# Optimization experiments

Hardware: AMD Instinct MI355X
Metric: run time of the kernel (lower is better)

Reference implementation:

```python
import jax, jax.numpy as jnp
import numpy as np

SEQ, B, IN, H, L = 512, 64, 128, 256, 6
STDV = 1.0 / (H ** 0.5)


def setup_inputs() -> dict:
    key = jax.random.key(0)
    ks = jax.random.split(key, 7)
    return {
        "x": jax.random.normal(ks[0], (SEQ, B, IN), jnp.float32),
        "h0": jax.random.normal(ks[1], (L, B, H), jnp.float32),
        "w_ih0": jax.random.uniform(ks[2], (3 * H, IN), jnp.float32, -STDV, STDV),
        "w_ih_rest": jax.random.uniform(ks[3], (L - 1, 3 * H, H), jnp.float32, -STDV, STDV),
        "w_hh": jax.random.uniform(ks[4], (L, 3 * H, H), jnp.float32, -STDV, STDV),
        "b_ih": jax.random.uniform(ks[5], (L, 3 * H), jnp.float32, -STDV, STDV),
        "b_hh": jax.random.uniform(ks[6], (L, 3 * H), jnp.float32, -STDV, STDV),
    }


def _gru_layer(x, h0, w_ih, w_hh, b_ih, b_hh):
    # Precompute input-side gate projections for all timesteps: (S, B, 3H)
    xg = jnp.einsum("sbi,gi->sbg", x, w_ih) + b_ih

    def step(h, xg_t):
        hg = h @ w_hh.T + b_hh  # (B, 3H)
        xr, xz, xn = jnp.split(xg_t, 3, axis=-1)
        hr, hz, hn = jnp.split(hg, 3, axis=-1)
        r = jax.nn.sigmoid(xr + hr)
        z = jax.nn.sigmoid(xz + hz)
        n = jnp.tanh(xn + r * hn)
        h_new = (1.0 - z) * n + z * h
        return h_new, h_new

    h_n, ys = jax.lax.scan(step, h0, xg)
    return ys, h_n


def reference(x, h0, w_ih0, w_ih_rest, w_hh, b_ih, b_hh):
    cur = x
    h_finals = []
    for i in range(L):
        w_ih = w_ih0 if i == 0 else w_ih_rest[i - 1]
        cur, h_n = _gru_layer(cur, h0[i], w_ih, w_hh[i], b_ih[i], b_hh[i])
        h_finals.append(h_n)
    return cur, jnp.stack(h_finals, axis=0)
```

## Files before the change

kernel.cpp:

```cpp
#include <hip/hip_runtime.h>

#define SEQ 512
#define BB 64
#define IN_DIM 128
#define HH 256
#define NL 6
#define G3 768
#define KT 16
#define SA 520
#define CUS_PER_LAYER 16
#define JPC 16
#define RD 4
#define RING_ELEMS (BB*HH)

typedef short short8 __attribute__((ext_vector_type(8)));
typedef short short4v __attribute__((ext_vector_type(4)));
typedef float f32x4 __attribute__((ext_vector_type(4)));

#define FLAGS_OFF_B (NL*RD*RING_ELEMS*2)
#define NFLAG_INTS  (NL*16 + 16)

__device__ __forceinline__ short f2bf(float f) {
    unsigned u = __builtin_bit_cast(unsigned, f);
    u += 0x7fffu + ((u >> 16) & 1u);
    return (short)(u >> 16);
}
__device__ __forceinline__ float sigm(float v) { return __fdividef(1.f, 1.f + __expf(-v)); }
__device__ __forceinline__ float tanh_f(float v) { float e = __expf(2.f * v); return 1.f - __fdividef(2.f, e + 1.f); }

__global__ __launch_bounds__(256, 1) void gru_persist(
    const float* __restrict__ x, const float* __restrict__ h0,
    const float* __restrict__ w_ih0, const float* __restrict__ w_ih_rest,
    const float* __restrict__ w_hh, const float* __restrict__ b_ih,
    const float* __restrict__ b_hh, float* __restrict__ y,
    short* __restrict__ ring, int* __restrict__ flags)
{
    extern __shared__ char dynpad[];
    (void)dynpad;

    const int tid = threadIdx.x;
    const unsigned long long ddl = __builtin_amdgcn_s_memrealtime() + 1000000000ull;

    const int xcc = __builtin_amdgcn_s_getreg(20 | (31 << 11)) & 0xf;
    if (xcc >= NL) return;
    __shared__ int s_slot;
    int* tickets = flags + NL * 16;
    if (tid == 0) s_slot = __hip_atomic_fetch_add(&tickets[xcc], 1, __ATOMIC_RELAXED, __HIP_MEMORY_SCOPE_AGENT);
    __syncthreads();
    const int slot = s_slot;
    if (slot >= CUS_PER_LAYER) return;

    const int l = xcc;
    const int jbase = slot * JPC;
    const int lane = tid & 63;
    const int wave = tid >> 6;
    const int q = lane >> 4;
    const int jj = lane & 15;
    const int jrow = jbase + jj;

    #define SQF(L) (flags + (L) * 16)

    __shared__ short sAm[64 * SA];
    __shared__ float sH[64 * 17];

    short* ring_init = ring + (l * RD + 3) * RING_ELEMS;
    for (int i = tid; i < BB * JPC; i += 256) {
        int b = i >> 4, j2 = i & 15;
        float v = h0[(size_t)l * BB * HH + b * HH + jbase + j2];
        sH[b * 17 + j2] = v;
        ring_init[b * HH + jbase + j2] = f2bf(v);
    }
    __syncthreads();
    if (tid == 0)
        __hip_atomic_store(&SQF(l)[slot], 1, __ATOMIC_RELEASE, __HIP_MEMORY_SCOPE_AGENT);

    if (l == 0) {
        short8 z8 = {};
        for (int i = tid; i < 64 * 16; i += 256) {
            int row = i >> 4, c8 = (i & 15) * 8;
            *reinterpret_cast<short8*>(&sAm[row * SA + 384 + c8]) = z8;
        }
    }

    const int KIN = (l == 0) ? IN_DIM : HH;
    const float* wih = (l == 0) ? w_ih0 : (w_ih_rest + (size_t)(l - 1) * G3 * HH);
    const float* whh = w_hh + (size_t)l * G3 * HH;
    const int kq = q * 8;
    short8 Breg[3 * KT];
    #pragma unroll
    for (int g = 0; g < 3; ++g) {
        const int row = g * HH + jrow;
        #pragma unroll
        for (int kt = 0; kt < KT; ++kt) {
            int k = kt * 32 + kq;
            short8 v = {};
            const float* p = nullptr;
            if (k < KIN)            p = wih + (size_t)row * KIN + k;
            else if (k < KIN + HH)  p = whh + (size_t)row * HH + (k - KIN);
            if (p) {
                float4 a = *(const float4*)p;
                float4 c = *(const float4*)(p + 4);
                v[0] = f2bf(a.x); v[1] = f2bf(a.y); v[2] = f2bf(a.z); v[3] = f2bf(a.w);
                v[4] = f2bf(c.x); v[5] = f2bf(c.y); v[6] = f2bf(c.z); v[7] = f2bf(c.w);
            }
            Breg[g * KT + kt] = v;
        }
    }
    const float bsr = b_ih[l * G3 + jrow] + b_hh[l * G3 + jrow];
    const float bsz = b_ih[l * G3 + HH + jrow] + b_hh[l * G3 + HH + jrow];
    const float bin_ = b_ih[l * G3 + 2 * HH + jrow];
    const float bhn_ = b_hh[l * G3 + 2 * HH + jrow];

    const int ksplit = (l == 0) ? 4 : 8;
    const int Mbase = wave * 16;
    const int aoff = (Mbase + jj) * SA + kq;

    int* paddr = SQF(l) + jj;
    bool pactive = false;
    int tshift = 0;
    if (wave == 0) {
        if (q == 0)      { paddr = SQF(l) + jj;     tshift = 1;  pactive = true; }
        else if (q == 1) { if (l > 0)      { paddr = SQF(l - 1) + jj; tshift = 2;  pactive = true; } }
        else if (q == 2) { if (l < NL - 1) { paddr = SQF(l + 1) + jj; tshift = -2; pactive = true; } }
    }

    for (int t = 0; t < SEQ; ++t) {
        if (wave == 0) {
            const int target = t + tshift;
            int iter = 0;
            for (;;) {
                int v = __hip_atomic_load(paddr, __ATOMIC_RELAXED, __HIP_MEMORY_SCOPE_AGENT);
                bool ok = (!pactive) || (v >= target);
                if (__ballot(ok) == 0xFFFFFFFFFFFFFFFFull) break;
                if (((++iter) & 63) == 0 && __builtin_amdgcn_s_memrealtime() > ddl) break;
            }
            __builtin_amdgcn_fence(__ATOMIC_ACQUIRE, "agent");
        }
        __syncthreads();

        {
            const short8* ph = (const short8*)((const char*)(ring + (l * RD + ((t + 3) & 3)) * RING_ELEMS) + tid * 128);
            short8 h0v = ph[0], h1v = ph[1], h2v = ph[2], h3v = ph[3];
            short8 h4v = ph[4], h5v = ph[5], h6v = ph[6], h7v = ph[7];
            short* dh = &sAm[(tid >> 2) * SA + KIN + (tid & 3) * 64];
            if (l == 0) {
                const float* xt = x + (size_t)t * BB * IN_DIM;
                #pragma unroll
                for (int i = 0; i < 8; ++i) {
                    int c = tid + i * 256;
                    int row = c >> 5, col = (c & 31) * 4;
                    float4 vv = *(const float4*)(xt + row * IN_DIM + col);
                    short4v s;
                    s[0] = f2bf(vv.x); s[1] = f2bf(vv.y); s[2] = f2bf(vv.z); s[3] = f2bf(vv.w);
                    *reinterpret_cast<short4v*>(&sAm[row * SA + col]) = s;
                }
            } else {
                const short8* pf = (const short8*)((const char*)(ring + ((l - 1) * RD + (t & 3)) * RING_ELEMS) + tid * 128);
                short8 w0 = pf[0], w1 = pf[1], w2 = pf[2], w3 = pf[3];
                short8 w4 = pf[4], w5 = pf[5], w6 = pf[6], w7 = pf[7];
                short* dx = &sAm[(tid >> 2) * SA + (tid & 3) * 64];
                *(short8*)(dx + 0)  = w0; *(short8*)(dx + 8)  = w1;
                *(short8*)(dx + 16) = w2; *(short8*)(dx + 24) = w3;
                *(short8*)(dx + 32) = w4; *(short8*)(dx + 40) = w5;
                *(short8*)(dx + 48) = w6; *(short8*)(dx + 56) = w7;
            }
            *(short8*)(dh + 0)  = h0v; *(short8*)(dh + 8)  = h1v;
            *(short8*)(dh + 16) = h2v; *(short8*)(dh + 24) = h3v;
            *(short8*)(dh + 32) = h4v; *(short8*)(dh + 40) = h5v;
            *(short8*)(dh + 48) = h6v; *(short8*)(dh + 56) = h7v;
        }
        __syncthreads();

        f32x4 ax0 = {}, ax1 = {}, ax2 = {}, ah0 = {}, ah1 = {}, ah2 = {};
        #pragma unroll
        for (int kt = 0; kt < KT; ++kt) {
            short8 a = *reinterpret_cast<const short8*>(&sAm[aoff + kt * 32]);
            if (kt < ksplit) {
                ax0 = __builtin_amdgcn_mfma_f32_16x16x32_bf16(a, Breg[0 * KT + kt], ax0, 0, 0, 0);
                ax1 = __builtin_amdgcn_mfma_f32_16x16x32_bf16(a, Breg[1 * KT + kt], ax1, 0, 0, 0);
                ax2 = __builtin_amdgcn_mfma_f32_16x16x32_bf16(a, Breg[2 * KT + kt], ax2, 0, 0, 0);
            } else {
                ah0 = __builtin_amdgcn_mfma_f32_16x16x32_bf16(a, Breg[0 * KT + kt], ah0, 0, 0, 0);
                ah1 = __builtin_amdgcn_mfma_f32_16x16x32_bf16(a, Breg[1 * KT + kt], ah1, 0, 0, 0);
                ah2 = __builtin_amdgcn_mfma_f32_16x16x32_bf16(a, Breg[2 * KT + kt], ah2, 0, 0, 0);
            }
        }

        short* rdst = ring + (l * RD + (t & 3)) * RING_ELEMS;
        float* ydst = y + (size_t)t * BB * HH;
        #pragma unroll
        for (int r = 0; r < 4; ++r) {
            int b = Mbase + 4 * q + r;
            float ho = sH[b * 17 + jj];
            float rg = sigm(ax0[r] + ah0[r] + bsr);
            float zg = sigm(ax1[r] + ah1[r] + bsz);
            float ng = tanh_f(ax2[r] + bin_ + rg * (ah2[r] + bhn_));
            float hn = ng + zg * (ho - ng);
            sH[b * 17 + jj] = hn;
            rdst[b * HH + jrow] = f2bf(hn);
            if (l == NL - 1) ydst[b * HH + jrow] = hn;
        }
        __syncthreads();
        if (tid == 0)
            __hip_atomic_store(&SQF(l)[slot], t + 2, __ATOMIC_RELEASE, __HIP_MEMORY_SCOPE_AGENT);
    }

    for (int i = tid; i < BB * JPC; i += 256) {
        int b = i >> 4, j2 = i & 15;
        y[(size_t)SEQ * BB * HH + (size_t)l * BB * HH + b * HH + jbase + j2] = sH[b * 17 + j2];
    }
}

extern "C" void kernel_launch(void* const* d_in, const int* in_sizes, int n_in,
                              void* d_out, int out_size, void* d_ws, size_t ws_size,
                              hipStream_t stream) {
    (void)in_sizes; (void)n_in; (void)out_size; (void)ws_size;
    const float* x         = (const float*)d_in[0];
    const float* h0        = (const float*)d_in[1];
    const float* w_ih0     = (const float*)d_in[2];
    const float* w_ih_rest = (const float*)d_in[3];
    const float* w_hh      = (const float*)d_in[4];
    const float* b_ih      = (const float*)d_in[5];
    const float* b_hh      = (const float*)d_in[6];
    float* y = (float*)d_out;

    short* ring = (short*)d_ws;
    int* flags  = (int*)((char*)d_ws + FLAGS_OFF_B);

    (void)hipMemsetAsync(flags, 0, NFLAG_INTS * sizeof(int), stream);
    gru_persist<<<256, 256, 16384, stream>>>(
        x, h0, w_ih0, w_ih_rest, w_hh, b_ih, b_hh, y, ring, flags);
}
```

Baseline: 4.630 ms.

## Split layers by batch groups with streamed weight fragments and chunked inter-layer handoff

Replaces the per-layer column split (16 CUs each owning 16 hidden units, exchanging the full hidden state every step) with a batch split: 4 CUs per layer each own 16 batch rows and all hidden units. The recurrence then stays local, with no per-timestep cross-CU synchronisation. A prep kernel converts weights into MFMA-fragment-ordered bf16 that each step streams from global/L2 instead of holding them in registers. Layers hand off through a chunked ring of 8 timesteps with producer and consumer flags. Each step now re-reads the full weight set from cache, and fewer CUs are active.

```diff
diff --git a/kernel.cpp b/kernel.cpp
--- a/kernel.cpp
+++ b/kernel.cpp
@@ -6,19 +6,24 @@
 #define HH 256
 #define NL 6
 #define G3 768
-#define KT 16
 #define SA 520
-#define CUS_PER_LAYER 16
-#define JPC 16
-#define RD 4
-#define RING_ELEMS (BB*HH)
+#define GPL 4
+#define MB 16
+#define CHUNK 8
+#define NSLOT 4
 
 typedef short short8 __attribute__((ext_vector_type(8)));
 typedef short short4v __attribute__((ext_vector_type(4)));
 typedef float f32x4 __attribute__((ext_vector_type(4)));
 
-#define FLAGS_OFF_B (NL*RD*RING_ELEMS*2)
-#define NFLAG_INTS  (NL*16 + 16)
+#define L0_FRAGS (48*12)
+#define LN_FRAGS (48*16)
+#define TOT_FRAGS (L0_FRAGS + 5*LN_FRAGS)
+#define STREAM_SHORTS ((size_t)TOT_FRAGS*512)
+#define FR_SLOT_SH ((size_t)CHUNK*MB*HH)
+#define FR_TOTAL_SH ((size_t)5*GPL*NSLOT*FR_SLOT_SH)
+#define FLAGS_OFF_B ((STREAM_SHORTS + FR_TOTAL_SH)*2)
+#define NFLAG_INTS (16 + 2*NL*GPL*16)
 
 __device__ __forceinline__ short f2bf(float f) {
     unsigned u = __builtin_bit_cast(unsigned, f);
@@ -28,186 +33,193 @@
 __device__ __forceinline__ float sigm(float v) { return __fdividef(1.f, 1.f + __expf(-v)); }
 __device__ __forceinline__ float tanh_f(float v) { float e = __expf(2.f * v); return 1.f - __fdividef(2.f, e + 1.f); }
 
-__global__ __launch_bounds__(256, 1) void gru_persist(
+__device__ __forceinline__ void spin1(int* p, int target, unsigned long long ddl) {
+    if (__hip_atomic_load(p, __ATOMIC_RELAXED, __HIP_MEMORY_SCOPE_AGENT) >= target) return;
+    for (;;) {
+        __builtin_amdgcn_s_sleep(2);
+        if (__hip_atomic_load(p, __ATOMIC_RELAXED, __HIP_MEMORY_SCOPE_AGENT) >= target) return;
+        if (__builtin_amdgcn_s_memrealtime() > ddl) return;
+    }
+}
+
+__global__ __launch_bounds__(256) void prep_frags(
+    const float* __restrict__ w_ih0, const float* __restrict__ w_ih_rest,
+    const float* __restrict__ w_hh, short* __restrict__ stream)
+{
+    int id = blockIdx.x * 256 + threadIdx.x;
+    if (id >= TOT_FRAGS * 64) return;
+    int fid = id >> 6, lane = id & 63;
+    int l, rem, KIN;
+    if (fid < L0_FRAGS) { l = 0; rem = fid; KIN = IN_DIM; }
+    else { int z = fid - L0_FRAGS; l = 1 + z / LN_FRAGS; rem = z - (l - 1) * LN_FRAGS; KIN = HH; }
+    int kt = rem / 48, nt = rem % 48;
+    int jt = nt / 3, gate = nt - jt * 3;
+    int jj = lane & 15, q2 = lane >> 4;
+    int row = gate * HH + jt * 16 + jj;
+    int k0 = kt * 32 + q2 * 8;
+    const float* src;
+    if (k0 < KIN) {
+        src = (l == 0) ? (w_ih0 + (size_t)row * IN_DIM + k0)
+                       : (w_ih_rest + (size_t)(l - 1) * G3 * HH + (size_t)row * HH + k0);
+    } else {
+        src = w_hh + (size_t)l * G3 * HH + (size_t)row * HH + (k0 - KIN);
+    }
+    float4 a = *(const float4*)src;
+    float4 c = *(const float4*)(src + 4);
+    short8 v;
+    v[0] = f2bf(a.x); v[1] = f2bf(a.y); v[2] = f2bf(a.z); v[3] = f2bf(a.w);
+    v[4] = f2bf(c.x); v[5] = f2bf(c.y); v[6] = f2bf(c.z); v[7] = f2bf(c.w);
+    *((short8*)stream + (size_t)fid * 64 + lane) = v;
+}
+
+template<int KTL, int KS>
+__device__ __forceinline__ void compute_step(const short* sAm, const short8* bs,
+                                             int wave, int lane, f32x4* acc)
+{
+    const int arow = (lane & 15) * SA + ((lane >> 4) * 8);
+    const int w6 = wave * 6;
+    #pragma unroll
+    for (int kt = 0; kt < KTL; ++kt) {
+        short8 a = *reinterpret_cast<const short8*>(&sAm[arow + kt * 32]);
+        const short8* bp = bs + ((size_t)(kt * 48 + w6) * 64 + lane);
+        short8 b0 = bp[0 * 64], b1 = bp[1 * 64], b2 = bp[2 * 64];
+        short8 b3 = bp[3 * 64], b4 = bp[4 * 64], b5 = bp[5 * 64];
+        acc[0] = __builtin_amdgcn_mfma_f32_16x16x32_bf16(a, b0, acc[0], 0, 0, 0);
+        acc[1] = __builtin_amdgcn_mfma_f32_16x16x32_bf16(a, b1, acc[1], 0, 0, 0);
+        if (kt < KS) acc[2] = __builtin_amdgcn_mfma_f32_16x16x32_bf16(a, b2, acc[2], 0, 0, 0);
+        else         acc[3] = __builtin_amdgcn_mfma_f32_16x16x32_bf16(a, b2, acc[3], 0, 0, 0);
+        acc[4] = __builtin_amdgcn_mfma_f32_16x16x32_bf16(a, b3, acc[4], 0, 0, 0);
+        acc[5] = __builtin_amdgcn_mfma_f32_16x16x32_bf16(a, b4, acc[5], 0, 0, 0);
+        if (kt < KS) acc[6] = __builtin_amdgcn_mfma_f32_16x16x32_bf16(a, b5, acc[6], 0, 0, 0);
+        else         acc[7] = __builtin_amdgcn_mfma_f32_16x16x32_bf16(a, b5, acc[7], 0, 0, 0);
+    }
+}
+
+__global__ __launch_bounds__(512, 1) void gru_persist(
     const float* __restrict__ x, const float* __restrict__ h0,
-    const float* __restrict__ w_ih0, const float* __restrict__ w_ih_rest,
-    const float* __restrict__ w_hh, const float* __restrict__ b_ih,
-    const float* __restrict__ b_hh, float* __restrict__ y,
-    short* __restrict__ ring, int* __restrict__ flags)
+    const float* __restrict__ b_ih, const float* __restrict__ b_hh,
+    float* __restrict__ y, const short* __restrict__ stream,
+    short* __restrict__ fring, int* __restrict__ flags)
 {
-    extern __shared__ char dynpad[];
-    (void)dynpad;
-
+    extern __shared__ short sAm[];
     const int tid = threadIdx.x;
     const unsigned long long ddl = __builtin_amdgcn_s_memrealtime() + 1000000000ull;
 
     const int xcc = __builtin_amdgcn_s_getreg(20 | (31 << 11)) & 0xf;
     if (xcc >= NL) return;
     __shared__ int s_slot;
-    int* tickets = flags + NL * 16;
-    if (tid == 0) s_slot = __hip_atomic_fetch_add(&tickets[xcc], 1, __ATOMIC_RELAXED, __HIP_MEMORY_SCOPE_AGENT);
+    if (tid == 0) s_slot = __hip_atomic_fetch_add(&flags[xcc], 1, __ATOMIC_RELAXED, __HIP_MEMORY_SCOPE_AGENT);
     __syncthreads();
-    const int slot = s_slot;
-    if (slot >= CUS_PER_LAYER) return;
+    const int g = s_slot;
+    if (g >= GPL) return;
 
     const int l = xcc;
-    const int jbase = slot * JPC;
     const int lane = tid & 63;
     const int wave = tid >> 6;
     const int q = lane >> 4;
     const int jj = lane & 15;
-    const int jrow = jbase + jj;
-
-    #define SQF(L) (flags + (L) * 16)
-
-    __shared__ short sAm[64 * SA];
-    __shared__ float sH[64 * 17];
-
-    short* ring_init = ring + (l * RD + 3) * RING_ELEMS;
-    for (int i = tid; i < BB * JPC; i += 256) {
-        int b = i >> 4, j2 = i & 15;
-        float v = h0[(size_t)l * BB * HH + b * HH + jbase + j2];
-        sH[b * 17 + j2] = v;
-        ring_init[b * HH + jbase + j2] = f2bf(v);
-    }
-    __syncthreads();
-    if (tid == 0)
-        __hip_atomic_store(&SQF(l)[slot], 1, __ATOMIC_RELEASE, __HIP_MEMORY_SCOPE_AGENT);
-
-    if (l == 0) {
-        short8 z8 = {};
-        for (int i = tid; i < 64 * 16; i += 256) {
-            int row = i >> 4, c8 = (i & 15) * 8;
-            *reinterpret_cast<short8*>(&sAm[row * SA + 384 + c8]) = z8;
-        }
-    }
-
-    const int KIN = (l == 0) ? IN_DIM : HH;
-    const float* wih = (l == 0) ? w_ih0 : (w_ih_rest + (size_t)(l - 1) * G3 * HH);
-    const float* whh = w_hh + (size_t)l * G3 * HH;
-    const int kq = q * 8;
-    short8 Breg[3 * KT];
+    const int KINC = (l == 0) ? IN_DIM : HH;
+
+    int* seqf  = flags + 16 + (l * GPL + g) * 16;
+    int* cseqf = flags + 16 + NL * GPL * 16 + (l * GPL + g) * 16;
+    int* seq_prev  = flags + 16 + ((l - 1) * GPL + g) * 16;
+    int* cseq_next = flags + 16 + NL * GPL * 16 + ((l + 1) * GPL + g) * 16;
+
+    const short8* bs = (const short8*)stream + (size_t)((l == 0) ? 0 : (L0_FRAGS + (l - 1) * LN_FRAGS)) * 64;
+
+    float hcur[8];
+    float bR[2], bZ[2], bNx[2], bNh[2];
     #pragma unroll
-    for (int g = 0; g < 3; ++g) {
-        const int row = g * HH + jrow;
-        #pragma unroll
-        for (int kt = 0; kt < KT; ++kt) {
-            int k = kt * 32 + kq;
-            short8 v = {};
-            const float* p = nullptr;
-            if (k < KIN)            p = wih + (size_t)row * KIN + k;
-            else if (k < KIN + HH)  p = whh + (size_t)row * HH + (k - KIN);
-            if (p) {
-                float4 a = *(const float4*)p;
-                float4 c = *(const float4*)(p + 4);
-                v[0] = f2bf(a.x); v[1] = f2bf(a.y); v[2] = f2bf(a.z); v[3] = f2bf(a.w);
-                v[4] = f2bf(c.x); v[5] = f2bf(c.y); v[6] = f2bf(c.z); v[7] = f2bf(c.w);
-            }
-            Breg[g * KT + kt] = v;
-        }
-    }
-    const float bsr = b_ih[l * G3 + jrow] + b_hh[l * G3 + jrow];
-    const float bsz = b_ih[l * G3 + HH + jrow] + b_hh[l * G3 + HH + jrow];
-    const float bin_ = b_ih[l * G3 + 2 * HH + jrow];
-    const float bhn_ = b_hh[l * G3 + 2 * HH + jrow];
-
-    const int ksplit = (l == 0) ? 4 : 8;
-    const int Mbase = wave * 16;
-    const int aoff = (Mbase + jj) * SA + kq;
-
-    int* paddr = SQF(l) + jj;
-    bool pactive = false;
-    int tshift = 0;
-    if (wave == 0) {
-        if (q == 0)      { paddr = SQF(l) + jj;     tshift = 1;  pactive = true; }
-        else if (q == 1) { if (l > 0)      { paddr = SQF(l - 1) + jj; tshift = 2;  pactive = true; } }
-        else if (q == 2) { if (l < NL - 1) { paddr = SQF(l + 1) + jj; tshift = -2; pactive = true; } }
-    }
-
-    for (int t = 0; t < SEQ; ++t) {
-        if (wave == 0) {
-            const int target = t + tshift;
-            int iter = 0;
-            for (;;) {
-                int v = __hip_atomic_load(paddr, __ATOMIC_RELAXED, __HIP_MEMORY_SCOPE_AGENT);
-                bool ok = (!pactive) || (v >= target);
-                if (__ballot(ok) == 0xFFFFFFFFFFFFFFFFull) break;
-                if (((++iter) & 63) == 0 && __builtin_amdgcn_s_memrealtime() > ddl) break;
-            }
-            __builtin_amdgcn_fence(__ATOMIC_ACQUIRE, "agent");
-        }
-        __syncthreads();
-
-        {
-            const short8* ph = (const short8*)((const char*)(ring + (l * RD + ((t + 3) & 3)) * RING_ELEMS) + tid * 128);
-            short8 h0v = ph[0], h1v = ph[1], h2v = ph[2], h3v = ph[3];
-            short8 h4v = ph[4], h5v = ph[5], h6v = ph[6], h7v = ph[7];
-            short* dh = &sAm[(tid >> 2) * SA + KIN + (tid & 3) * 64];
-            if (l == 0) {
-                const float* xt = x + (size_t)t * BB * IN_DIM;
-                #pragma unroll
-                for (int i = 0; i < 8; ++i) {
-                    int c = tid + i * 256;
-                    int row = c >> 5, col = (c & 31) * 4;
-                    float4 vv = *(const float4*)(xt + row * IN_DIM + col);
-                    short4v s;
-                    s[0] = f2bf(vv.x); s[1] = f2bf(vv.y); s[2] = f2bf(vv.z); s[3] = f2bf(vv.w);
-                    *reinterpret_cast<short4v*>(&sAm[row * SA + col]) = s;
-                }
-            } else {
-                const short8* pf = (const short8*)((const char*)(ring + ((l - 1) * RD + (t & 3)) * RING_ELEMS) + tid * 128);
-                short8 w0 = pf[0], w1 = pf[1], w2 = pf[2], w3 = pf[3];
-                short8 w4 = pf[4], w5 = pf[5], w6 = pf[6], w7 = pf[7];
-                short* dx = &sAm[(tid >> 2) * SA + (tid & 3) * 64];
-                *(short8*)(dx + 0)  = w0; *(short8*)(dx + 8)  = w1;
-                *(short8*)(dx + 16) = w2; *(short8*)(dx + 24) = w3;
-                *(short8*)(dx + 32) = w4; *(short8*)(dx + 40) = w5;
-                *(short8*)(dx + 48) = w6; *(short8*)(dx + 56) = w7;
-            }
-            *(short8*)(dh + 0)  = h0v; *(short8*)(dh + 8)  = h1v;
-            *(short8*)(dh + 16) = h2v; *(short8*)(dh + 24) = h3v;
-            *(short8*)(dh + 32) = h4v; *(short8*)(dh + 40) = h5v;
-            *(short8*)(dh + 48) = h6v; *(short8*)(dh + 56) = h7v;
-        }
-        __syncthreads();
-
-        f32x4 ax0 = {}, ax1 = {}, ax2 = {}, ah0 = {}, ah1 = {}, ah2 = {};
-        #pragma unroll
-        for (int kt = 0; kt < KT; ++kt) {
-            short8 a = *reinterpret_cast<const short8*>(&sAm[aoff + kt * 32]);
-            if (kt < ksplit) {
-                ax0 = __builtin_amdgcn_mfma_f32_16x16x32_bf16(a, Breg[0 * KT + kt], ax0, 0, 0, 0);
-                ax1 = __builtin_amdgcn_mfma_f32_16x16x32_bf16(a, Breg[1 * KT + kt], ax1, 0, 0, 0);
-                ax2 = __builtin_amdgcn_mfma_f32_16x16x32_bf16(a, Breg[2 * KT + kt], ax2, 0, 0, 0);
-            } else {
-                ah0 = __builtin_amdgcn_mfma_f32_16x16x32_bf16(a, Breg[0 * KT + kt], ah0, 0, 0, 0);
-                ah1 = __builtin_amdgcn_mfma_f32_16x16x32_bf16(a, Breg[1 * KT + kt], ah1, 0, 0, 0);
-                ah2 = __builtin_amdgcn_mfma_f32_16x16x32_bf16(a, Breg[2 * KT + kt], ah2, 0, 0, 0);
-            }
-        }
-
-        short* rdst = ring + (l * RD + (t & 3)) * RING_ELEMS;
-        float* ydst = y + (size_t)t * BB * HH;
+    for (int jt2 = 0; jt2 < 2; ++jt2) {
+        int j = (2 * wave + jt2) * 16 + jj;
+        bR[jt2]  = b_ih[l * G3 + j] + b_hh[l * G3 + j];
+        bZ[jt2]  = b_ih[l * G3 + HH + j] + b_hh[l * G3 + HH + j];
+        bNx[jt2] = b_ih[l * G3 + 2 * HH + j];
+        bNh[jt2] = b_hh[l * G3 + 2 * HH + j];
         #pragma unroll
         for (int r = 0; r < 4; ++r) {
-            int b = Mbase + 4 * q + r;
-            float ho = sH[b * 17 + jj];
-            float rg = sigm(ax0[r] + ah0[r] + bsr);
-            float zg = sigm(ax1[r] + ah1[r] + bsz);
-            float ng = tanh_f(ax2[r] + bin_ + rg * (ah2[r] + bhn_));
-            float hn = ng + zg * (ho - ng);
-            sH[b * 17 + jj] = hn;
-            rdst[b * HH + jrow] = f2bf(hn);
-            if (l == NL - 1) ydst[b * HH + jrow] = hn;
+            int b = 4 * q + r;
+            float v = h0[((size_t)l * BB + g * MB + b) * HH + j];
+            hcur[jt2 * 4 + r] = v;
+        }
+    }
+    for (int i = tid; i < MB * HH; i += 512) {
+        int b = i >> 8, j = i & 255;
+        sAm[b * SA + KINC + j] = f2bf(h0[((size_t)l * BB + g * MB + b) * HH + j]);
+    }
+
+    for (int t = 0; t < SEQ; ++t) {
+        if ((t & 7) == 0) {
+            if (tid == 0) {
+                if (l > 0) spin1(seq_prev, t + CHUNK, ddl);
+                if (l < NL - 1 && t >= NSLOT * CHUNK) spin1(cseq_next, t - (NSLOT - 1) * CHUNK, ddl);
+            }
+            if (wave == 0) __builtin_amdgcn_fence(__ATOMIC_ACQUIRE, "agent");
+            __syncthreads();
+        }
+
+        const int slot = (t >> 3) & (NSLOT - 1);
+
+        if (l == 0) {
+            const float* xt = x + ((size_t)t * BB + g * MB) * IN_DIM;
+            int row = tid >> 5, col = (tid & 31) * 4;
+            float4 vv = *(const float4*)(xt + row * IN_DIM + col);
+            short4v s;
+            s[0] = f2bf(vv.x); s[1] = f2bf(vv.y); s[2] = f2bf(vv.z); s[3] = f2bf(vv.w);
+            *reinterpret_cast<short4v*>(&sAm[row * SA + col]) = s;
+        } else {
+            const short* frsrc = fring + (((size_t)((l - 1) * GPL + g) * NSLOT + slot)) * FR_SLOT_SH
+                               + (size_t)(t & 7) * MB * HH;
+            int row = tid >> 5, col = (tid & 31) * 8;
+            short8 v = *(const short8*)&frsrc[row * HH + col];
+            *reinterpret_cast<short8*>(&sAm[row * SA + col]) = v;
         }
         __syncthreads();
-        if (tid == 0)
-            __hip_atomic_store(&SQF(l)[slot], t + 2, __ATOMIC_RELEASE, __HIP_MEMORY_SCOPE_AGENT);
-    }
-
-    for (int i = tid; i < BB * JPC; i += 256) {
-        int b = i >> 4, j2 = i & 15;
-        y[(size_t)SEQ * BB * HH + (size_t)l * BB * HH + b * HH + jbase + j2] = sH[b * 17 + j2];
+
+        f32x4 acc[8] = {};
+        if (l == 0) compute_step<12, 4>(sAm, bs, wave, lane, acc);
+        else        compute_step<16, 8>(sAm, bs, wave, lane, acc);
+        __syncthreads();
+
+        short* frdst = fring + (((size_t)(l * GPL + g) * NSLOT + slot)) * FR_SLOT_SH
+                     + (size_t)(t & 7) * MB * HH;
+        float* ydst = y + (size_t)t * BB * HH + (size_t)g * MB * HH;
+        #pragma unroll
+        for (int jt2 = 0; jt2 < 2; ++jt2) {
+            int j = (2 * wave + jt2) * 16 + jj;
+            #pragma unroll
+            for (int r = 0; r < 4; ++r) {
+                int b = 4 * q + r;
+                float ho = hcur[jt2 * 4 + r];
+                float rg = sigm(acc[jt2 * 4 + 0][r] + bR[jt2]);
+                float zg = sigm(acc[jt2 * 4 + 1][r] + bZ[jt2]);
+                float ng = tanh_f(acc[jt2 * 4 + 2][r] + bNx[jt2] + rg * (acc[jt2 * 4 + 3][r] + bNh[jt2]));
+                float hn = ng + zg * (ho - ng);
+                hcur[jt2 * 4 + r] = hn;
+                short hb = f2bf(hn);
+                sAm[b * SA + KINC + j] = hb;
+                if (l < NL - 1) frdst[b * HH + j] = hb;
+                else            ydst[b * HH + j] = hn;
+            }
+        }
+        __syncthreads();
+
+        if ((t & 7) == 7 && tid == 0) {
+            if (l < NL - 1)
+                __hip_atomic_store(seqf, t + 1, __ATOMIC_RELEASE, __HIP_MEMORY_SCOPE_AGENT);
+            if (l > 0)
+                __hip_atomic_store(cseqf, t + 1, __ATOMIC_RELEASE, __HIP_MEMORY_SCOPE_AGENT);
+        }
+    }
+
+    #pragma unroll
+    for (int jt2 = 0; jt2 < 2; ++jt2) {
+        int j = (2 * wave + jt2) * 16 + jj;
+        #pragma unroll
+        for (int r = 0; r < 4; ++r) {
+            int b = 4 * q + r;
+            y[(size_t)SEQ * BB * HH + (size_t)l * BB * HH + (size_t)(g * MB + b) * HH + j] = hcur[jt2 * 4 + r];
+        }
     }
 }
 
@@ -224,10 +236,11 @@
     const float* b_hh      = (const float*)d_in[6];
     float* y = (float*)d_out;
 
-    short* ring = (short*)d_ws;
-    int* flags  = (int*)((char*)d_ws + FLAGS_OFF_B);
+    short* wstream = (short*)d_ws;
+    short* fring   = wstream + STREAM_SHORTS;
+    int*   flags   = (int*)((char*)d_ws + FLAGS_OFF_B);
 
     (void)hipMemsetAsync(flags, 0, NFLAG_INTS * sizeof(int), stream);
-    gru_persist<<<256, 256, 16384, stream>>>(
-        x, h0, w_ih0, w_ih_rest, w_hh, b_ih, b_hh, y, ring, flags);
-}
+    prep_frags<<<(TOT_FRAGS * 64) / 256, 256, 0, stream>>>(w_ih0, w_ih_rest, w_hh, wstream);
+    gru_persist<<<256, 512, 65536, stream>>>(x, h0, b_ih, b_hh, y, wstream, fring, flags);
+}
```

Measured after the change: 4.837 ms. 4.5% more time.

## Split GRU into recurrent and input-projection workgroups with chunked pipelining

Applied to the files above, without the earlier changes.

Restructures the persistent kernel so each layer has 4 recurrent workgroups, each owning 16 batch rows and all 256 hidden units with W_hh held in registers and LDS. It also has 16 projection workgroups that compute the input gate projections for 8-timestep chunks into a global double buffer. Synchronisation moves from per-timestep flags across 16 CUs to per-chunk flags between the producer and consumer roles. The aim is to take the input GEMM off the serial recurrence path and cut cross-CU handshakes per step. The cost is more workspace traffic, heavy register use at 512 threads, and a bf16 rounding of the stored gate projections.

```diff
diff --git a/kernel.cpp b/kernel.cpp
--- a/kernel.cpp
+++ b/kernel.cpp
@@ -6,208 +6,272 @@
 #define HH 256
 #define NL 6
 #define G3 768
-#define KT 16
-#define SA 520
-#define CUS_PER_LAYER 16
-#define JPC 16
-#define RD 4
-#define RING_ELEMS (BB*HH)
+#define CHUNK 8
+#define NCH (SEQ/CHUNK)
+#define FSTR 16
 
 typedef short short8 __attribute__((ext_vector_type(8)));
 typedef short short4v __attribute__((ext_vector_type(4)));
 typedef float f32x4 __attribute__((ext_vector_type(4)));
 
-#define FLAGS_OFF_B (NL*RD*RING_ELEMS*2)
-#define NFLAG_INTS  (NL*16 + 16)
+#define FR_SH ((size_t)5*4*CHUNK*BB*HH)
+#define XG_SH ((size_t)NL*2*CHUNK*G3*BB)
+#define FLAGS_OFF_B ((FR_SH + XG_SH)*2)
+#define NFLAG_INTS (16 + (24 + 96)*FSTR)
 
 __device__ __forceinline__ short f2bf(float f) {
     unsigned u = __builtin_bit_cast(unsigned, f);
     u += 0x7fffu + ((u >> 16) & 1u);
     return (short)(u >> 16);
 }
+__device__ __forceinline__ float b2f(short s) {
+    unsigned u = ((unsigned)(unsigned short)s) << 16;
+    return __builtin_bit_cast(float, u);
+}
 __device__ __forceinline__ float sigm(float v) { return __fdividef(1.f, 1.f + __expf(-v)); }
 __device__ __forceinline__ float tanh_f(float v) { float e = __expf(2.f * v); return 1.f - __fdividef(2.f, e + 1.f); }
 
-__global__ __launch_bounds__(256, 1) void gru_persist(
+__device__ __forceinline__ short8 pack_row(const float* p) {
+    float4 a = *(const float4*)p;
+    float4 c = *(const float4*)(p + 4);
+    short8 v;
+    v[0] = f2bf(a.x); v[1] = f2bf(a.y); v[2] = f2bf(a.z); v[3] = f2bf(a.w);
+    v[4] = f2bf(c.x); v[5] = f2bf(c.y); v[6] = f2bf(c.z); v[7] = f2bf(c.w);
+    return v;
+}
+
+__global__ __launch_bounds__(512, 1) void gru_persist(
     const float* __restrict__ x, const float* __restrict__ h0,
     const float* __restrict__ w_ih0, const float* __restrict__ w_ih_rest,
     const float* __restrict__ w_hh, const float* __restrict__ b_ih,
     const float* __restrict__ b_hh, float* __restrict__ y,
-    short* __restrict__ ring, int* __restrict__ flags)
+    short* __restrict__ fring, short* __restrict__ xg, int* __restrict__ flags)
 {
-    extern __shared__ char dynpad[];
-    (void)dynpad;
-
+    extern __shared__ char smem[];
     const int tid = threadIdx.x;
-    const unsigned long long ddl = __builtin_amdgcn_s_memrealtime() + 1000000000ull;
+    const unsigned long long ddl = __builtin_amdgcn_s_memrealtime() + 800000000ull;
 
     const int xcc = __builtin_amdgcn_s_getreg(20 | (31 << 11)) & 0xf;
     if (xcc >= NL) return;
     __shared__ int s_slot;
-    int* tickets = flags + NL * 16;
-    if (tid == 0) s_slot = __hip_atomic_fetch_add(&tickets[xcc], 1, __ATOMIC_RELAXED, __HIP_MEMORY_SCOPE_AGENT);
+    if (tid == 0) s_slot = __hip_atomic_fetch_add(&flags[xcc], 1, __ATOMIC_RELAXED, __HIP_MEMORY_SCOPE_AGENT);
     __syncthreads();
     const int slot = s_slot;
-    if (slot >= CUS_PER_LAYER) return;
+    if (slot >= 20) return;
 
     const int l = xcc;
-    const int jbase = slot * JPC;
     const int lane = tid & 63;
     const int wave = tid >> 6;
     const int q = lane >> 4;
     const int jj = lane & 15;
-    const int jrow = jbase + jj;
-
-    #define SQF(L) (flags + (L) * 16)
-
-    __shared__ short sAm[64 * SA];
-    __shared__ float sH[64 * 17];
-
-    short* ring_init = ring + (l * RD + 3) * RING_ELEMS;
-    for (int i = tid; i < BB * JPC; i += 256) {
-        int b = i >> 4, j2 = i & 15;
-        float v = h0[(size_t)l * BB * HH + b * HH + jbase + j2];
-        sH[b * 17 + j2] = v;
-        ring_init[b * HH + jbase + j2] = f2bf(v);
-    }
-    __syncthreads();
-    if (tid == 0)
-        __hip_atomic_store(&SQF(l)[slot], 1, __ATOMIC_RELEASE, __HIP_MEMORY_SCOPE_AGENT);
-
-    if (l == 0) {
-        short8 z8 = {};
-        for (int i = tid; i < 64 * 16; i += 256) {
-            int row = i >> 4, c8 = (i & 15) * 8;
-            *reinterpret_cast<short8*>(&sAm[row * SA + 384 + c8]) = z8;
-        }
-    }
-
-    const int KIN = (l == 0) ? IN_DIM : HH;
-    const float* wih = (l == 0) ? w_ih0 : (w_ih_rest + (size_t)(l - 1) * G3 * HH);
-    const float* whh = w_hh + (size_t)l * G3 * HH;
-    const int kq = q * 8;
-    short8 Breg[3 * KT];
-    #pragma unroll
-    for (int g = 0; g < 3; ++g) {
-        const int row = g * HH + jrow;
-        #pragma unroll
-        for (int kt = 0; kt < KT; ++kt) {
-            int k = kt * 32 + kq;
-            short8 v = {};
-            const float* p = nullptr;
-            if (k < KIN)            p = wih + (size_t)row * KIN + k;
-            else if (k < KIN + HH)  p = whh + (size_t)row * HH + (k - KIN);
-            if (p) {
-                float4 a = *(const float4*)p;
-                float4 c = *(const float4*)(p + 4);
-                v[0] = f2bf(a.x); v[1] = f2bf(a.y); v[2] = f2bf(a.z); v[3] = f2bf(a.w);
-                v[4] = f2bf(c.x); v[5] = f2bf(c.y); v[6] = f2bf(c.z); v[7] = f2bf(c.w);
-            }
-            Breg[g * KT + kt] = v;
-        }
-    }
-    const float bsr = b_ih[l * G3 + jrow] + b_hh[l * G3 + jrow];
-    const float bsz = b_ih[l * G3 + HH + jrow] + b_hh[l * G3 + HH + jrow];
-    const float bin_ = b_ih[l * G3 + 2 * HH + jrow];
-    const float bhn_ = b_hh[l * G3 + 2 * HH + jrow];
-
-    const int ksplit = (l == 0) ? 4 : 8;
-    const int Mbase = wave * 16;
-    const int aoff = (Mbase + jj) * SA + kq;
-
-    int* paddr = SQF(l) + jj;
-    bool pactive = false;
-    int tshift = 0;
-    if (wave == 0) {
-        if (q == 0)      { paddr = SQF(l) + jj;     tshift = 1;  pactive = true; }
-        else if (q == 1) { if (l > 0)      { paddr = SQF(l - 1) + jj; tshift = 2;  pactive = true; } }
-        else if (q == 2) { if (l < NL - 1) { paddr = SQF(l + 1) + jj; tshift = -2; pactive = true; } }
-    }
-
-    for (int t = 0; t < SEQ; ++t) {
-        if (wave == 0) {
-            const int target = t + tshift;
-            int iter = 0;
-            for (;;) {
-                int v = __hip_atomic_load(paddr, __ATOMIC_RELAXED, __HIP_MEMORY_SCOPE_AGENT);
-                bool ok = (!pactive) || (v >= target);
-                if (__ballot(ok) == 0xFFFFFFFFFFFFFFFFull) break;
-                if (((++iter) & 63) == 0 && __builtin_amdgcn_s_memrealtime() > ddl) break;
-            }
-            __builtin_amdgcn_fence(__ATOMIC_ACQUIRE, "agent");
+
+    int* recF  = flags + 16;
+    int* projF = flags + 16 + 24 * FSTR;
+
+    if (slot < 4) {
+        const int g = slot;
+        char* sWn = smem;
+        char* sHB = smem + 131072;
+
+        const float* whh = w_hh + (size_t)l * G3 * HH;
+        short8 Wreg[4][8];
+        #pragma unroll
+        for (int i = 0; i < 4; ++i) {
+            int row = (i >> 1) * HH + 32 * wave + 16 * (i & 1) + jj;
+            #pragma unroll
+            for (int kt = 0; kt < 8; ++kt)
+                Wreg[i][kt] = pack_row(whh + (size_t)row * HH + kt * 32 + q * 8);
+        }
+        #pragma unroll
+        for (int i2 = 0; i2 < 2; ++i2) {
+            int row = 512 + 32 * wave + 16 * i2 + jj;
+            #pragma unroll
+            for (int kt = 0; kt < 8; ++kt) {
+                short8 v = pack_row(whh + (size_t)row * HH + kt * 32 + q * 8);
+                *(short8*)(sWn + ((size_t)(wave * 2 + i2) * 8 + kt) * 1024 + lane * 16) = v;
+            }
+        }
+        float bhr[2], bhz[2], bhn2[2];
+        #pragma unroll
+        for (int jt2 = 0; jt2 < 2; ++jt2) {
+            int j = 32 * wave + 16 * jt2 + jj;
+            bhr[jt2]  = b_hh[l * G3 + j];
+            bhz[jt2]  = b_hh[l * G3 + 256 + j];
+            bhn2[jt2] = b_hh[l * G3 + 512 + j];
+        }
+        float hcur[2][4];
+        #pragma unroll
+        for (int jt2 = 0; jt2 < 2; ++jt2) {
+            int j = 32 * wave + 16 * jt2 + jj;
+            #pragma unroll
+            for (int r = 0; r < 4; ++r)
+                hcur[jt2][r] = h0[((size_t)l * BB + 16 * g + 4 * q + r) * HH + j];
+        }
+        for (int i = tid; i < 16 * 256; i += 512) {
+            int b = i >> 8, j = i & 255;
+            short hb = f2bf(h0[((size_t)l * BB + 16 * g + b) * HH + j]);
+            *(short*)(sHB + b * 512 + ((2 * j) ^ ((b & 7) << 4))) = hb;
         }
         __syncthreads();
 
-        {
-            const short8* ph = (const short8*)((const char*)(ring + (l * RD + ((t + 3) & 3)) * RING_ELEMS) + tid * 128);
-            short8 h0v = ph[0], h1v = ph[1], h2v = ph[2], h3v = ph[3];
-            short8 h4v = ph[4], h5v = ph[5], h6v = ph[6], h7v = ph[7];
-            short* dh = &sAm[(tid >> 2) * SA + KIN + (tid & 3) * 64];
-            if (l == 0) {
-                const float* xt = x + (size_t)t * BB * IN_DIM;
+        for (int c = 0; c < NCH; ++c) {
+            if (wave == 0) {
+                const int* pa = nullptr; int tgt = 0;
+                if (lane < 8) { pa = &projF[(l * 16 + 2 * lane + (g >> 1)) * FSTR]; tgt = c + 1; }
+                else if (lane < 16 && l < NL - 1) { pa = &projF[((l + 1) * 16 + 2 * (lane - 8) + (g >> 1)) * FSTR]; tgt = c - 3; }
+                int it = 0;
+                for (;;) {
+                    bool ok = true;
+                    if (pa) ok = __hip_atomic_load((int*)pa, __ATOMIC_RELAXED, __HIP_MEMORY_SCOPE_AGENT) >= tgt;
+                    if (__ballot(ok) == ~0ull) break;
+                    __builtin_amdgcn_s_sleep(1);
+                    if (((++it) & 63) == 0 && __builtin_amdgcn_s_memrealtime() > ddl) break;
+                }
+                __builtin_amdgcn_fence(__ATOMIC_ACQUIRE, "agent");
+            }
+            __syncthreads();
+
+            const short* xgc = xg + ((size_t)(l * 2 + (c & 1)) * CHUNK) * G3 * BB;
+            short* frc = (l < NL - 1) ? fring + ((size_t)(l * 4 + (c & 3)) * CHUNK) * BB * HH : nullptr;
+
+            for (int ts = 0; ts < CHUNK; ++ts) {
+                const int t = c * CHUNK + ts;
+                const int cur = t & 1, nxt = cur ^ 1;
+                f32x4 acc[6] = {};
                 #pragma unroll
-                for (int i = 0; i < 8; ++i) {
-                    int c = tid + i * 256;
-                    int row = c >> 5, col = (c & 31) * 4;
-                    float4 vv = *(const float4*)(xt + row * IN_DIM + col);
-                    short4v s;
-                    s[0] = f2bf(vv.x); s[1] = f2bf(vv.y); s[2] = f2bf(vv.z); s[3] = f2bf(vv.w);
-                    *reinterpret_cast<short4v*>(&sAm[row * SA + col]) = s;
-                }
-            } else {
-                const short8* pf = (const short8*)((const char*)(ring + ((l - 1) * RD + (t & 3)) * RING_ELEMS) + tid * 128);
-                short8 w0 = pf[0], w1 = pf[1], w2 = pf[2], w3 = pf[3];
-                short8 w4 = pf[4], w5 = pf[5], w6 = pf[6], w7 = pf[7];
-                short* dx = &sAm[(tid >> 2) * SA + (tid & 3) * 64];
-                *(short8*)(dx + 0)  = w0; *(short8*)(dx + 8)  = w1;
-                *(short8*)(dx + 16) = w2; *(short8*)(dx + 24) = w3;
-                *(short8*)(dx + 32) = w4; *(short8*)(dx + 40) = w5;
-                *(short8*)(dx + 48) = w6; *(short8*)(dx + 56) = w7;
-            }
-            *(short8*)(dh + 0)  = h0v; *(short8*)(dh + 8)  = h1v;
-            *(short8*)(dh + 16) = h2v; *(short8*)(dh + 24) = h3v;
-            *(short8*)(dh + 32) = h4v; *(short8*)(dh + 40) = h5v;
-            *(short8*)(dh + 48) = h6v; *(short8*)(dh + 56) = h7v;
-        }
+                for (int kt = 0; kt < 8; ++kt) {
+                    short8 af = *(const short8*)(sHB + cur * 8192 + (lane & 15) * 512
+                                 + ((kt * 64 + q * 16) ^ ((lane & 7) << 4)));
+                    acc[0] = __builtin_amdgcn_mfma_f32_16x16x32_bf16(af, Wreg[0][kt], acc[0], 0, 0, 0);
+                    acc[1] = __builtin_amdgcn_mfma_f32_16x16x32_bf16(af, Wreg[1][kt], acc[1], 0, 0, 0);
+                    acc[2] = __builtin_amdgcn_mfma_f32_16x16x32_bf16(af, Wreg[2][kt], acc[2], 0, 0, 0);
+                    acc[3] = __builtin_amdgcn_mfma_f32_16x16x32_bf16(af, Wreg[3][kt], acc[3], 0, 0, 0);
+                    short8 w4 = *(const short8*)(sWn + ((size_t)(wave * 2 + 0) * 8 + kt) * 1024 + lane * 16);
+                    short8 w5 = *(const short8*)(sWn + ((size_t)(wave * 2 + 1) * 8 + kt) * 1024 + lane * 16);
+                    acc[4] = __builtin_amdgcn_mfma_f32_16x16x32_bf16(af, w4, acc[4], 0, 0, 0);
+                    acc[5] = __builtin_amdgcn_mfma_f32_16x16x32_bf16(af, w5, acc[5], 0, 0, 0);
+                }
+                const short* xgt = xgc + (size_t)ts * G3 * BB;
+                float* ydst = y + (size_t)t * BB * HH;
+                #pragma unroll
+                for (int jt2 = 0; jt2 < 2; ++jt2) {
+                    int j = 32 * wave + 16 * jt2 + jj;
+                    short4v xr = *(const short4v*)(xgt + (size_t)j * BB + 16 * g + 4 * q);
+                    short4v xz = *(const short4v*)(xgt + (size_t)(256 + j) * BB + 16 * g + 4 * q);
+                    short4v xn = *(const short4v*)(xgt + (size_t)(512 + j) * BB + 16 * g + 4 * q);
+                    #pragma unroll
+                    for (int r = 0; r < 4; ++r) {
+                        int b = 4 * q + r;
+                        float rg = sigm(acc[jt2][r] + b2f(xr[r]) + bhr[jt2]);
+                        float zg = sigm(acc[2 + jt2][r] + b2f(xz[r]) + bhz[jt2]);
+                        float ng = tanh_f(b2f(xn[r]) + rg * (acc[4 + jt2][r] + bhn2[jt2]));
+                        float hn = ng + zg * (hcur[jt2][r] - ng);
+                        hcur[jt2][r] = hn;
+                        short hb = f2bf(hn);
+                        *(short*)(sHB + nxt * 8192 + b * 512 + ((2 * j) ^ ((b & 7) << 4))) = hb;
+                        if (l < NL - 1) frc[((size_t)ts * BB + 16 * g + b) * HH + j] = hb;
+                        else            ydst[((size_t)16 * g + b) * HH + j] = hn;
+                    }
+                }
+                __syncthreads();
+            }
+            if (tid == 0)
+                __hip_atomic_store(&recF[(l * 4 + g) * FSTR], c + 1, __ATOMIC_RELEASE, __HIP_MEMORY_SCOPE_AGENT);
+        }
+        #pragma unroll
+        for (int jt2 = 0; jt2 < 2; ++jt2) {
+            int j = 32 * wave + 16 * jt2 + jj;
+            #pragma unroll
+            for (int r = 0; r < 4; ++r)
+                y[(size_t)SEQ * BB * HH + (size_t)l * BB * HH + ((size_t)16 * g + 4 * q + r) * HH + j] = hcur[jt2][r];
+        }
+    } else {
+        const int p = slot - 4;
+        const int t_p = p >> 1;
+        const int bh = p & 1;
+        const int KIN = (l == 0) ? IN_DIM : HH;
+        const int KTp = (l == 0) ? 4 : 8;
+        char* sWp = smem;
+
+        const float* wih = (l == 0) ? w_ih0 : (w_ih_rest + (size_t)(l - 1) * G3 * HH);
+        short8 Wp[4][8];
+        #pragma unroll
+        for (int i = 0; i < 4; ++i) {
+            int row = (6 * wave + i) * 16 + jj;
+            for (int kt = 0; kt < KTp; ++kt)
+                Wp[i][kt] = pack_row(wih + (size_t)row * KIN + kt * 32 + q * 8);
+        }
+        #pragma unroll
+        for (int i2 = 0; i2 < 2; ++i2) {
+            int row = (6 * wave + 4 + i2) * 16 + jj;
+            for (int kt = 0; kt < KTp; ++kt) {
+                short8 v = pack_row(wih + (size_t)row * KIN + kt * 32 + q * 8);
+                *(short8*)(sWp + ((size_t)(wave * 2 + i2) * 8 + kt) * 1024 + lane * 16) = v;
+            }
+        }
+        float bias[6];
+        #pragma unroll
+        for (int i = 0; i < 6; ++i)
+            bias[i] = b_ih[l * G3 + (6 * wave + i) * 16 + jj];
         __syncthreads();
 
-        f32x4 ax0 = {}, ax1 = {}, ax2 = {}, ah0 = {}, ah1 = {}, ah2 = {};
-        #pragma unroll
-        for (int kt = 0; kt < KT; ++kt) {
-            short8 a = *reinterpret_cast<const short8*>(&sAm[aoff + kt * 32]);
-            if (kt < ksplit) {
-                ax0 = __builtin_amdgcn_mfma_f32_16x16x32_bf16(a, Breg[0 * KT + kt], ax0, 0, 0, 0);
-                ax1 = __builtin_amdgcn_mfma_f32_16x16x32_bf16(a, Breg[1 * KT + kt], ax1, 0, 0, 0);
-                ax2 = __builtin_amdgcn_mfma_f32_16x16x32_bf16(a, Breg[2 * KT + kt], ax2, 0, 0, 0);
-            } else {
-                ah0 = __builtin_amdgcn_mfma_f32_16x16x32_bf16(a, Breg[0 * KT + kt], ah0, 0, 0, 0);
-                ah1 = __builtin_amdgcn_mfma_f32_16x16x32_bf16(a, Breg[1 * KT + kt], ah1, 0, 0, 0);
-                ah2 = __builtin_amdgcn_mfma_f32_16x16x32_bf16(a, Breg[2 * KT + kt], ah2, 0, 0, 0);
-            }
-        }
-
-        short* rdst = ring + (l * RD + (t & 3)) * RING_ELEMS;
-        float* ydst = y + (size_t)t * BB * HH;
-        #pragma unroll
-        for (int r = 0; r < 4; ++r) {
-            int b = Mbase + 4 * q + r;
-            float ho = sH[b * 17 + jj];
-            float rg = sigm(ax0[r] + ah0[r] + bsr);
-            float zg = sigm(ax1[r] + ah1[r] + bsz);
-            float ng = tanh_f(ax2[r] + bin_ + rg * (ah2[r] + bhn_));
-            float hn = ng + zg * (ho - ng);
-            sH[b * 17 + jj] = hn;
-            rdst[b * HH + jrow] = f2bf(hn);
-            if (l == NL - 1) ydst[b * HH + jrow] = hn;
-        }
-        __syncthreads();
-        if (tid == 0)
-            __hip_atomic_store(&SQF(l)[slot], t + 2, __ATOMIC_RELEASE, __HIP_MEMORY_SCOPE_AGENT);
-    }
-
-    for (int i = tid; i < BB * JPC; i += 256) {
-        int b = i >> 4, j2 = i & 15;
-        y[(size_t)SEQ * BB * HH + (size_t)l * BB * HH + b * HH + jbase + j2] = sH[b * 17 + j2];
+        for (int c = 0; c < NCH; ++c) {
+            if (wave == 0) {
+                const int* pa = nullptr; int tgt = 0;
+                if (lane < 2) { if (l > 0) { pa = &recF[((l - 1) * 4 + 2 * bh + lane) * FSTR]; tgt = c + 1; } }
+                else if (lane < 4) { pa = &recF[(l * 4 + 2 * bh + (lane - 2)) * FSTR]; tgt = c - 1; }
+                int it = 0;
+                for (;;) {
+                    bool ok = true;
+                    if (pa) ok = __hip_atomic_load((int*)pa, __ATOMIC_RELAXED, __HIP_MEMORY_SCOPE_AGENT) >= tgt;
+                    if (__ballot(ok) == ~0ull) break;
+                    __builtin_amdgcn_s_sleep(1);
+                    if (((++it) & 63) == 0 && __builtin_amdgcn_s_memrealtime() > ddl) break;
+                }
+                __builtin_amdgcn_fence(__ATOMIC_ACQUIRE, "agent");
+            }
+            __syncthreads();
+
+            short* xgd = xg + ((size_t)(l * 2 + (c & 1)) * CHUNK + t_p) * G3 * BB;
+            const short* frs = (l > 0)
+                ? fring + ((size_t)((l - 1) * 4 + (c & 3)) * CHUNK + t_p) * BB * HH : nullptr;
+
+            #pragma unroll
+            for (int mt2 = 0; mt2 < 2; ++mt2) {
+                const int bgl = 32 * bh + 16 * mt2 + (lane & 15);
+                f32x4 acc[6] = {};
+                for (int kt = 0; kt < KTp; ++kt) {
+                    short8 af;
+                    if (l == 0) {
+                        const float* ap = x + ((size_t)(c * CHUNK + t_p) * BB + bgl) * IN_DIM + kt * 32 + q * 8;
+                        af = pack_row(ap);
+                    } else {
+                        af = *(const short8*)(frs + (size_t)bgl * HH + kt * 32 + q * 8);
+                    }
+                    acc[0] = __builtin_amdgcn_mfma_f32_16x16x32_bf16(af, Wp[0][kt], acc[0], 0, 0, 0);
+                    acc[1] = __builtin_amdgcn_mfma_f32_16x16x32_bf16(af, Wp[1][kt], acc[1], 0, 0, 0);
+                    acc[2] = __builtin_amdgcn_mfma_f32_16x16x32_bf16(af, Wp[2][kt], acc[2], 0, 0, 0);
+                    acc[3] = __builtin_amdgcn_mfma_f32_16x16x32_bf16(af, Wp[3][kt], acc[3], 0, 0, 0);
+                    short8 w4 = *(const short8*)(sWp + ((size_t)(wave * 2 + 0) * 8 + kt) * 1024 + lane * 16);
+                    short8 w5 = *(const short8*)(sWp + ((size_t)(wave * 2 + 1) * 8 + kt) * 1024 + lane * 16);
+                    acc[4] = __builtin_amdgcn_mfma_f32_16x16x32_bf16(af, w4, acc[4], 0, 0, 0);
+                    acc[5] = __builtin_amdgcn_mfma_f32_16x16x32_bf16(af, w5, acc[5], 0, 0, 0);
+                }
+                #pragma unroll
+                for (int i = 0; i < 6; ++i) {
+                    int j = (6 * wave + i) * 16 + jj;
+                    short4v o;
+                    o[0] = f2bf(acc[i][0] + bias[i]);
+                    o[1] = f2bf(acc[i][1] + bias[i]);
+                    o[2] = f2bf(acc[i][2] + bias[i]);
+                    o[3] = f2bf(acc[i][3] + bias[i]);
+                    *(short4v*)(xgd + (size_t)j * BB + 32 * bh + 16 * mt2 + 4 * q) = o;
+                }
+            }
+            __syncthreads();
+            if (tid == 0)
+                __hip_atomic_store(&projF[(l * 16 + p) * FSTR], c + 1, __ATOMIC_RELEASE, __HIP_MEMORY_SCOPE_AGENT);
+        }
     }
 }
 
@@ -224,10 +288,11 @@
     const float* b_hh      = (const float*)d_in[6];
     float* y = (float*)d_out;
 
-    short* ring = (short*)d_ws;
-    int* flags  = (int*)((char*)d_ws + FLAGS_OFF_B);
+    short* fring = (short*)d_ws;
+    short* xgb   = fring + FR_SH;
+    int*   flags = (int*)((char*)d_ws + FLAGS_OFF_B);
 
     (void)hipMemsetAsync(flags, 0, NFLAG_INTS * sizeof(int), stream);
-    gru_persist<<<256, 256, 16384, stream>>>(
-        x, h0, w_ih0, w_ih_rest, w_hh, b_ih, b_hh, y, ring, flags);
-}
+    gru_persist<<<256, 512, 147456, stream>>>(
+        x, h0, w_ih0, w_ih_rest, w_hh, b_ih, b_hh, y, fring, xgb, flags);
+}
```

Result: no change. 4.673 ms (+0.9%).
